# Optimization experiments

Hardware: AMD Instinct MI355X
Metric: run time of the kernel (lower is better)

## Reference

```python
import jax, jax.numpy as jnp
import numpy as np
import math

B, S, HID = 16, 1024, 1024
H, D = 16, 64  # heads, head_dim
WINDOW = 512  # pos bias length = 2*WINDOW+1 = 1025


def setup_inputs() -> dict:
    key = jax.random.key(0)
    ks = jax.random.split(key, 12)
    xav = lambda k, shp: jax.random.uniform(k, shp, jnp.float32, -1.0, 1.0) * math.sqrt(6.0 / (shp[0] + shp[1]))
    return {
        "hidden_states": jax.random.normal(ks[0], (B, S, HID), jnp.float32),
        "Wq": xav(ks[1], (HID, HID)), "bq": jnp.zeros((HID,), jnp.float32),
        "Wk": xav(ks[2], (HID, HID)), "bk": jnp.zeros((HID,), jnp.float32),
        "Wv": xav(ks[3], (HID, HID)), "bv": jnp.zeros((HID,), jnp.float32),
        "Wo": xav(ks[4], (HID, HID)), "bo": jnp.zeros((HID,), jnp.float32),
        "W_pe": xav(ks[5], (HID, 1)), "b_pe": jnp.zeros((HID,), jnp.float32),
        "pos_bias": 0.02 * jax.random.normal(ks[6], (1, H, 1, 2 * WINDOW + 1), jnp.float32),
        "clip_info": 0,
    }


def reference(hidden_states, Wq, bq, Wk, bk, Wv, bv, Wo, bo, W_pe, b_pe, pos_bias, clip_info):
    b, s, hid = hidden_states.shape
    mid = s // 2
    # relative positions in [-1, 1), shape [s, 1]
    positions = ((jnp.arange(s) - mid).astype(jnp.float32) / (mid + 1e-6))[:, None]
    pos_emb = positions @ W_pe.T + b_pe  # [s, hid]
    hs = hidden_states + pos_emb

    def heads(x):
        return x.reshape(b, s, H, D).transpose(0, 2, 1, 3)  # [b, H, s, D]

    q = heads(hs @ Wq.T + bq)
    k = heads(hs @ Wk.T + bk)
    v = heads(hs @ Wv.T + bv)

    scores = jnp.einsum("bhqd,bhkd->bhqk", q, k) / math.sqrt(D)
    scores = scores + pos_bias[:, :, :, :s]  # broadcast learned window bias over batch and query
    probs = jax.nn.softmax(scores, axis=-1)  # dropout is identity in eval mode
    ctx = jnp.einsum("bhqk,bhkd->bhqd", probs, v)
    ctx = ctx.transpose(0, 2, 1, 3).reshape(b, s, hid)
    return ctx @ Wo.T + bo
```

## Files before the change

kernel.cpp:

```cpp
#include <hip/hip_runtime.h>
#include <hip/hip_bf16.h>
#include <stdint.h>

#define BATCH 16
#define SEQ   1024
#define HIDN  1024
#define NH    16
#define HD    64
#define PBSTRIDE 1025

#define TS  64
#define AST 76

#define KSCL 0.18033688f
#define L2E  1.44269504f
#define MSUB 11.54156032f

#if __has_builtin(__builtin_amdgcn_exp2f)
#define EXP2(x) __builtin_amdgcn_exp2f(x)
#else
#define EXP2(x) exp2f(x)
#endif

typedef __attribute__((ext_vector_type(8))) short short8;
typedef __attribute__((ext_vector_type(4))) short short4v;
typedef __attribute__((ext_vector_type(4))) float f32x4;

__device__ __forceinline__ float bf2f(short x) {
    unsigned int u = ((unsigned int)(unsigned short)x) << 16;
    union { unsigned int u; float f; } c; c.u = u; return c.f;
}
__device__ __forceinline__ short f2bf(float f) {
    union { float f; unsigned int u; } c; c.f = f;
    unsigned int r = c.u + 0x7FFFu + ((c.u >> 16) & 1u);
    return (short)(r >> 16);
}
__device__ __forceinline__ short f2bf_fast(float f) {
    __hip_bfloat16 h = __float2bfloat16(f);
    return *reinterpret_cast<short*>(&h);
}

typedef __attribute__((address_space(1))) void gvoid;
typedef __attribute__((address_space(3))) void svoid;
__device__ __forceinline__ void gload_lds16(const void* g, void* l) {
    __builtin_amdgcn_global_load_lds((gvoid*)g, (svoid*)l, 16, 0, 0);
}

__global__ void convw4_k(const float* __restrict__ s0, const float* __restrict__ s1,
                         const float* __restrict__ s2, const float* __restrict__ s3,
                         short* __restrict__ d0, short* __restrict__ d1,
                         short* __restrict__ d2, short* __restrict__ d3) {
    const float* src = (blockIdx.y == 0) ? s0 : (blockIdx.y == 1) ? s1 : (blockIdx.y == 2) ? s2 : s3;
    short* dst       = (blockIdx.y == 0) ? d0 : (blockIdx.y == 1) ? d1 : (blockIdx.y == 2) ? d2 : d3;
    const float scl  = (blockIdx.y == 1) ? KSCL : 1.0f;
    int i = (blockIdx.x * 256 + threadIdx.x) * 4;
    float4 f = *(const float4*)(src + i);
    short4v o;
    o[0] = f2bf(f.x * scl); o[1] = f2bf(f.y * scl); o[2] = f2bf(f.z * scl); o[3] = f2bf(f.w * scl);
    *(short4v*)(dst + i) = o;
}

__global__ void convb_k(const float* __restrict__ b0, const float* __restrict__ b1,
                        const float* __restrict__ b2, float* __restrict__ fb) {
    int i = blockIdx.x * 256 + threadIdx.x;
    const float* s = (i < 1024) ? b0 : (i < 2048) ? b1 : b2;
    float scl = (i >= 1024 && i < 2048) ? KSCL : 1.0f;
    fb[i] = s[i & 1023] * scl;
}

__global__ void posemb_k(const float* __restrict__ hid, const float* __restrict__ wpe,
                         const float* __restrict__ bpe, short* __restrict__ hs) {
    long long idx = (long long)blockIdx.x * blockDim.x + threadIdx.x;
    long long base = idx * 8;
    int c = (int)(base & (HIDN - 1));
    int s = (int)((base >> 10) & (SEQ - 1));
    float pos = (float)(s - 512) * (1.0f / 512.0f);
    float4 h0 = *(const float4*)(hid + base);
    float4 h1 = *(const float4*)(hid + base + 4);
    float4 w0 = *(const float4*)(wpe + c);
    float4 w1 = *(const float4*)(wpe + c + 4);
    float4 b0 = *(const float4*)(bpe + c);
    float4 b1 = *(const float4*)(bpe + c + 4);
    short8 ov;
    ov[0] = f2bf(h0.x + pos * w0.x + b0.x);
    ov[1] = f2bf(h0.y + pos * w0.y + b0.y);
    ov[2] = f2bf(h0.z + pos * w0.z + b0.z);
    ov[3] = f2bf(h0.w + pos * w0.w + b0.w);
    ov[4] = f2bf(h1.x + pos * w1.x + b1.x);
    ov[5] = f2bf(h1.y + pos * w1.y + b1.y);
    ov[6] = f2bf(h1.z + pos * w1.z + b1.z);
    ov[7] = f2bf(h1.w + pos * w1.w + b1.w);
    *(short8*)(hs + base) = ov;
}

__global__ __launch_bounds__(256) void gemm_qkv(const short* __restrict__ A,
                                                const short* __restrict__ W,
                                                const float* __restrict__ fb,
                                                short* __restrict__ q,
                                                short* __restrict__ k,
                                                short* __restrict__ vt) {
    __shared__ __align__(16) short Als[128 * 64];
    __shared__ __align__(16) short Bls[128 * 64];
    const int tid  = threadIdx.x;
    const int lane = tid & 63;
    const int w    = tid >> 6;
    const int wr   = w >> 1, wc = w & 1;
    const int d0   = blockIdx.x;
    const int xcd  = d0 & 7;
    const int idx  = d0 >> 3;
    const int tx   = idx >> 4;
    const int ty   = xcd * 16 + (idx & 15);
    const int tm   = ty * 128;
    const int tn   = tx * 128;

    f32x4 acc[4][4] = {};

    const int srow = w * 32 + (lane >> 3);
    const int scol = ((lane & 7) ^ (lane >> 3)) * 8;
    const long long a_base = (long long)(tm + srow) * 1024 + scol;
    const long long b_base = (long long)(tn + srow) * 1024 + scol;
    char* alds = (char*)Als + w * 4096;
    char* blds = (char*)Bls + w * 4096;

    const int fr  = lane & 15;
    const int fg8 = (lane >> 4) * 8;
    const int frx = (lane & 7) * 8;

    for (int k0 = 0; k0 < 1024; k0 += 64) {
#pragma unroll
        for (int c = 0; c < 4; ++c) {
            gload_lds16((const void*)(A + a_base + (long long)c * 8 * 1024 + k0), alds + c * 1024);
            gload_lds16((const void*)(W + b_base + (long long)c * 8 * 1024 + k0), blds + c * 1024);
        }
        __syncthreads();
#pragma unroll
        for (int ks = 0; ks < 2; ++ks) {
            short8 af[4], bfr[4];
#pragma unroll
            for (int r = 0; r < 4; ++r) {
                af[r]  = *(const short8*)(Als + (wr * 64 + r * 16 + fr) * 64 + ((ks * 32 + fg8) ^ frx));
                bfr[r] = *(const short8*)(Bls + (wc * 64 + r * 16 + fr) * 64 + ((ks * 32 + fg8) ^ frx));
            }
#pragma unroll
            for (int mi = 0; mi < 4; ++mi)
#pragma unroll
                for (int ni = 0; ni < 4; ++ni)
                    acc[mi][ni] = __builtin_amdgcn_mfma_f32_16x16x32_bf16(af[mi], bfr[ni], acc[mi][ni], 0, 0, 0);
        }
        __syncthreads();
    }

    const int which = tn >> 10;
    short* dst = (which == 0) ? q : (which == 1) ? k : vt;
    const int g4 = (lane >> 4) * 4;
#pragma unroll
    for (int ni = 0; ni < 4; ++ni) {
        int col = tn + wc * 64 + ni * 16 + fr;
        int cc  = col & 1023;
        int h   = cc >> 6, d = cc & 63;
        float bv = fb[col];
#pragma unroll
        for (int mi = 0; mi < 4; ++mi) {
#pragma unroll
            for (int r = 0; r < 4; ++r) {
                int row = tm + wr * 64 + mi * 16 + g4 + r;
                int b = row >> 10, s = row & 1023;
                short o = f2bf(acc[mi][ni][r] + bv);
                if (which < 2)
                    dst[(((long long)(b * NH + h) * SEQ + s) << 6) + d] = o;
                else
                    dst[((long long)(b * NH + h) * HD + d) * SEQ + s] = o;
            }
        }
    }
}

__global__ __launch_bounds__(256) void gemm_out(const short* __restrict__ A,
                                                const short* __restrict__ W,
                                                const float* __restrict__ bias,
                                                float* __restrict__ Cout) {
    __shared__ __align__(16) short Als[128 * 64];
    __shared__ __align__(16) short Bls[128 * 64];
    const int tid  = threadIdx.x;
    const int lane = tid & 63;
    const int w    = tid >> 6;
    const int wr   = w >> 1, wc = w & 1;
    const int d0   = blockIdx.x;
    const int xcd  = d0 & 7;
    const int idx  = d0 >> 3;
    const int tx   = idx >> 4;
    const int ty   = xcd * 16 + (idx & 15);
    const int tm   = ty * 128;
    const int tn   = tx * 128;

    f32x4 acc[4][4] = {};

    const int srow = w * 32 + (lane >> 3);
    const int scol = ((lane & 7) ^ (lane >> 3)) * 8;
    const long long a_base = (long long)(tm + srow) * 1024 + scol;
    const long long b_base = (long long)(tn + srow) * 1024 + scol;
    char* alds = (char*)Als + w * 4096;
    char* blds = (char*)Bls + w * 4096;

    const int fr  = lane & 15;
    const int fg8 = (lane >> 4) * 8;
    const int frx = (lane & 7) * 8;

    for (int k0 = 0; k0 < 1024; k0 += 64) {
#pragma unroll
        for (int c = 0; c < 4; ++c) {
            gload_lds16((const void*)(A + a_base + (long long)c * 8 * 1024 + k0), alds + c * 1024);
            gload_lds16((const void*)(W + b_base + (long long)c * 8 * 1024 + k0), blds + c * 1024);
        }
        __syncthreads();
#pragma unroll
        for (int ks = 0; ks < 2; ++ks) {
            short8 af[4], bfr[4];
#pragma unroll
            for (int r = 0; r < 4; ++r) {
                af[r]  = *(const short8*)(Als + (wr * 64 + r * 16 + fr) * 64 + ((ks * 32 + fg8) ^ frx));
                bfr[r] = *(const short8*)(Bls + (wc * 64 + r * 16 + fr) * 64 + ((ks * 32 + fg8) ^ frx));
            }
#pragma unroll
            for (int mi = 0; mi < 4; ++mi)
#pragma unroll
                for (int ni = 0; ni < 4; ++ni)
                    acc[mi][ni] = __builtin_amdgcn_mfma_f32_16x16x32_bf16(af[mi], bfr[ni], acc[mi][ni], 0, 0, 0);
        }
        __syncthreads();
    }

    const int g4 = (lane >> 4) * 4;
#pragma unroll
    for (int ni = 0; ni < 4; ++ni) {
        int col = tn + wc * 64 + ni * 16 + fr;
        float bv = bias[col];
#pragma unroll
        for (int mi = 0; mi < 4; ++mi)
#pragma unroll
            for (int r = 0; r < 4; ++r) {
                int row = tm + wr * 64 + mi * 16 + g4 + r;
                Cout[(long long)row * 1024 + col] = acc[mi][ni][r] + bv;
            }
    }
}

__global__ __launch_bounds__(256) void attn_k(const short* __restrict__ Q,
                                              const short* __restrict__ Kg,
                                              const short* __restrict__ Vt,
                                              const float* __restrict__ pbias,
                                              short* __restrict__ ctx) {
    __shared__ __align__(16) short Kls[2][64 * TS];
    __shared__ __align__(16) short Vls[2][64 * TS];
    __shared__ __align__(16) short Pls[4 * 32 * AST];

    const int tid  = threadIdx.x;
    const int lane = tid & 63;
    const int w    = tid >> 6;
    const int d0   = blockIdx.x;
    const int bh   = (d0 & 7) * 32 + (d0 >> 6);
    const int qt   = (d0 >> 3) & 7;
    const int h    = bh & (NH - 1);
    const long long base = (long long)bh * (SEQ * HD);

    const int fr = lane & 15;
    const int fg = lane >> 4;

    const int trow = w * 16 + (lane >> 3);
    const int scol = ((lane & 7) ^ (lane >> 3)) * 8;
    const int ldso = w * 1024;
    const long long kg0 = base + (long long)trow * HD + scol;
    const long long vg0 = base + (long long)trow * SEQ + scol;

    short8 qf[2][2];
#pragma unroll
    for (int mi = 0; mi < 2; ++mi)
#pragma unroll
        for (int ks = 0; ks < 2; ++ks)
            qf[mi][ks] = *(const short8*)(Q + base + (long long)(qt * 128 + w * 32 + mi * 16 + fr) * HD + ks * 32 + fg * 8);

    f32x4 o[2][4] = {};
    f32x4 osum[2] = {};
    short8 vones;
#pragma unroll
    for (int j = 0; j < 8; ++j) vones[j] = (short)0x3F80;

    short* Pw = Pls + w * 32 * AST;
    const float* pbh = pbias + h * PBSTRIDE;
    const int swc = (fr & 7) << 3;

    {
        const short* ks0 = Kg + kg0;
        const short* vs0 = Vt + vg0;
        gload_lds16(ks0,           Kls[0] + ldso);
        gload_lds16(ks0 + 8 * HD,  Kls[0] + ldso + 512);
        gload_lds16(vs0,           Vls[0] + ldso);
        gload_lds16(vs0 + 8 * SEQ, Vls[0] + ldso + 512);
    }
    float pbm[4];
#pragma unroll
    for (int ni = 0; ni < 4; ++ni)
        pbm[ni] = fmaf(pbh[ni * 16 + fr], L2E, -MSUB);
    asm volatile("s_waitcnt vmcnt(0)" ::: "memory");
    __syncthreads();

    int cur = 0;
    for (int kt = 0; kt < 16; ++kt) {
        if (kt < 15) {
            const int nb = cur ^ 1;
            const short* ks0 = Kg + kg0 + (long long)((kt + 1) * 64) * HD;
            const short* vs0 = Vt + vg0 + (kt + 1) * 64;
            gload_lds16(ks0,           Kls[nb] + ldso);
            gload_lds16(ks0 + 8 * HD,  Kls[nb] + ldso + 512);
            gload_lds16(vs0,           Vls[nb] + ldso);
            gload_lds16(vs0 + 8 * SEQ, Vls[nb] + ldso + 512);
        }

        f32x4 sc[2][4];
#pragma unroll
        for (int mi = 0; mi < 2; ++mi)
#pragma unroll
            for (int ni = 0; ni < 4; ++ni)
                sc[mi][ni] = (f32x4){pbm[ni], pbm[ni], pbm[ni], pbm[ni]};
        __builtin_amdgcn_s_setprio(1);
#pragma unroll
        for (int ks = 0; ks < 2; ++ks) {
#pragma unroll
            for (int ni = 0; ni < 4; ++ni) {
                short8 kb = *(const short8*)(Kls[cur] + (ni * 16 + fr) * TS + ((ks * 32 + fg * 8) ^ swc));
#pragma unroll
                for (int mi = 0; mi < 2; ++mi)
                    sc[mi][ni] = __builtin_amdgcn_mfma_f32_16x16x32_bf16(qf[mi][ks], kb, sc[mi][ni], 0, 0, 0);
            }
        }
        __builtin_amdgcn_s_setprio(0);

#pragma unroll
        for (int mi = 0; mi < 2; ++mi)
#pragma unroll
            for (int ni = 0; ni < 4; ++ni)
#pragma unroll
                for (int r = 0; r < 4; ++r)
                    Pw[(mi * 16 + fg * 4 + r) * AST + ni * 16 + fr] =
                        f2bf_fast(EXP2(sc[mi][ni][r]));

        {
            const int nkt = (kt + 1) & 15;
#pragma unroll
            for (int ni = 0; ni < 4; ++ni)
                pbm[ni] = fmaf(pbh[nkt * 64 + ni * 16 + fr], L2E, -MSUB);
        }

        __builtin_amdgcn_s_setprio(1);
#pragma unroll
        for (int ks = 0; ks < 2; ++ks) {
            short8 pa[2];
#pragma unroll
            for (int mi = 0; mi < 2; ++mi)
                pa[mi] = *(const short8*)(Pw + (mi * 16 + fr) * AST + ks * 32 + fg * 8);
            osum[0] = __builtin_amdgcn_mfma_f32_16x16x32_bf16(pa[0], vones, osum[0], 0, 0, 0);
            osum[1] = __builtin_amdgcn_mfma_f32_16x16x32_bf16(pa[1], vones, osum[1], 0, 0, 0);
#pragma unroll
            for (int di = 0; di < 4; ++di) {
                short8 vb = *(const short8*)(Vls[cur] + (di * 16 + fr) * TS + ((ks * 32 + fg * 8) ^ swc));
#pragma unroll
                for (int mi = 0; mi < 2; ++mi)
                    o[mi][di] = __builtin_amdgcn_mfma_f32_16x16x32_bf16(pa[mi], vb, o[mi][di], 0, 0, 0);
            }
        }
        __builtin_amdgcn_s_setprio(0);

        asm volatile("s_waitcnt vmcnt(0)" ::: "memory");
        __syncthreads();
        cur ^= 1;
    }

    const int b = bh >> 4;
#pragma unroll
    for (int mi = 0; mi < 2; ++mi) {
#pragma unroll
        for (int r = 0; r < 4; ++r) {
            float inv = 1.0f / osum[mi][r];
            int srow = qt * 128 + w * 32 + mi * 16 + fg * 4 + r;
#pragma unroll
            for (int di = 0; di < 4; ++di) {
                int d = di * 16 + fr;
                ctx[(long long)(b * SEQ + srow) * HIDN + h * HD + d] = f2bf(o[mi][di][r] * inv);
            }
        }
    }
}

extern "C" void kernel_launch(void* const* d_in, const int* in_sizes, int n_in,
                              void* d_out, int out_size, void* d_ws, size_t ws_size,
                              hipStream_t stream) {
    const float* hid  = (const float*)d_in[0];
    const float* Wq   = (const float*)d_in[1];
    const float* bq   = (const float*)d_in[2];
    const float* Wk   = (const float*)d_in[3];
    const float* bk   = (const float*)d_in[4];
    const float* Wv   = (const float*)d_in[5];
    const float* bv   = (const float*)d_in[6];
    const float* Wo   = (const float*)d_in[7];
    const float* bo   = (const float*)d_in[8];
    const float* Wpe  = (const float*)d_in[9];
    const float* bpe  = (const float*)d_in[10];
    const float* pbias = (const float*)d_in[11];

    const long long NE = (long long)BATCH * SEQ * HIDN;
    const long long WSZ = (long long)HIDN * HIDN;

    short* hs   = (short*)d_ws;
    short* vt   = hs + NE;
    short* Wcq  = vt + NE;
    short* Wck  = Wcq + WSZ;
    short* Wcv  = Wck + WSZ;
    short* Wco  = Wcv + WSZ;
    float* fb   = (float*)(Wco + WSZ);
    short* q    = (short*)d_out;
    short* k    = q + NE;
    short* ctx  = hs;

    posemb_k<<<(int)(NE / 8 / 256), 256, 0, stream>>>(hid, Wpe, bpe, hs);
    convw4_k<<<dim3((int)(WSZ / 4 / 256), 4), 256, 0, stream>>>(Wq, Wk, Wv, Wo, Wcq, Wck, Wcv, Wco);
    convb_k<<<12, 256, 0, stream>>>(bq, bk, bv, fb);

    gemm_qkv<<<3072, 256, 0, stream>>>(hs, Wcq, fb, q, k, vt);

    attn_k<<<2048, 256, 0, stream>>>(q, k, vt, pbias, ctx);

    gemm_out<<<1024, 256, 0, stream>>>(ctx, Wco, bo, (float*)d_out);
}
```

Before: 352.5 us.

## Double-buffer LDS tiles in QKV and output GEMMs; vectorize V-transpose store

Both projection GEMMs now allocate two LDS buffers per operand. They prefetch the next K-tile via global-to-LDS loads while MFMAs run on the current tile, so load latency overlaps compute instead of being serialized behind a barrier. The QKV epilogue is split by destination, and the transposed V output now writes four consecutive sequence elements as one packed store instead of scalar stores. LDS use per block doubles, which can lower occupancy. Correctness relies on the barrier at the end of each iteration also draining the outstanding async loads.

Result: faster. 338.2 us (-4.1%).

```diff
diff --git a/kernel.cpp b/kernel.cpp
--- a/kernel.cpp
+++ b/kernel.cpp
@@ -99,8 +99,8 @@
                                                 short* __restrict__ q,
                                                 short* __restrict__ k,
                                                 short* __restrict__ vt) {
-    __shared__ __align__(16) short Als[128 * 64];
-    __shared__ __align__(16) short Bls[128 * 64];
+    __shared__ __align__(16) short Als[2][128 * 64];
+    __shared__ __align__(16) short Bls[2][128 * 64];
     const int tid  = threadIdx.x;
     const int lane = tid & 63;
     const int w    = tid >> 6;
@@ -119,27 +119,39 @@
     const int scol = ((lane & 7) ^ (lane >> 3)) * 8;
     const long long a_base = (long long)(tm + srow) * 1024 + scol;
     const long long b_base = (long long)(tn + srow) * 1024 + scol;
-    char* alds = (char*)Als + w * 4096;
-    char* blds = (char*)Bls + w * 4096;
+    const int ldsw = w * 4096;
 
     const int fr  = lane & 15;
     const int fg8 = (lane >> 4) * 8;
     const int frx = (lane & 7) * 8;
 
+#pragma unroll
+    for (int c = 0; c < 4; ++c) {
+        gload_lds16((const void*)(A + a_base + (long long)c * 8 * 1024), (char*)Als[0] + ldsw + c * 1024);
+        gload_lds16((const void*)(W + b_base + (long long)c * 8 * 1024), (char*)Bls[0] + ldsw + c * 1024);
+    }
+    asm volatile("s_waitcnt vmcnt(0)" ::: "memory");
+    __syncthreads();
+
+    int cur = 0;
     for (int k0 = 0; k0 < 1024; k0 += 64) {
-#pragma unroll
-        for (int c = 0; c < 4; ++c) {
-            gload_lds16((const void*)(A + a_base + (long long)c * 8 * 1024 + k0), alds + c * 1024);
-            gload_lds16((const void*)(W + b_base + (long long)c * 8 * 1024 + k0), blds + c * 1024);
-        }
-        __syncthreads();
+        if (k0 + 64 < 1024) {
+            const int nb = cur ^ 1;
+#pragma unroll
+            for (int c = 0; c < 4; ++c) {
+                gload_lds16((const void*)(A + a_base + (long long)c * 8 * 1024 + k0 + 64),
+                            (char*)Als[nb] + ldsw + c * 1024);
+                gload_lds16((const void*)(W + b_base + (long long)c * 8 * 1024 + k0 + 64),
+                            (char*)Bls[nb] + ldsw + c * 1024);
+            }
+        }
 #pragma unroll
         for (int ks = 0; ks < 2; ++ks) {
             short8 af[4], bfr[4];
 #pragma unroll
             for (int r = 0; r < 4; ++r) {
-                af[r]  = *(const short8*)(Als + (wr * 64 + r * 16 + fr) * 64 + ((ks * 32 + fg8) ^ frx));
-                bfr[r] = *(const short8*)(Bls + (wc * 64 + r * 16 + fr) * 64 + ((ks * 32 + fg8) ^ frx));
+                af[r]  = *(const short8*)(Als[cur] + (wr * 64 + r * 16 + fr) * 64 + ((ks * 32 + fg8) ^ frx));
+                bfr[r] = *(const short8*)(Bls[cur] + (wc * 64 + r * 16 + fr) * 64 + ((ks * 32 + fg8) ^ frx));
             }
 #pragma unroll
             for (int mi = 0; mi < 4; ++mi)
@@ -148,28 +160,44 @@
                     acc[mi][ni] = __builtin_amdgcn_mfma_f32_16x16x32_bf16(af[mi], bfr[ni], acc[mi][ni], 0, 0, 0);
         }
         __syncthreads();
+        cur ^= 1;
     }
 
     const int which = tn >> 10;
-    short* dst = (which == 0) ? q : (which == 1) ? k : vt;
     const int g4 = (lane >> 4) * 4;
-#pragma unroll
-    for (int ni = 0; ni < 4; ++ni) {
-        int col = tn + wc * 64 + ni * 16 + fr;
-        int cc  = col & 1023;
-        int h   = cc >> 6, d = cc & 63;
-        float bv = fb[col];
-#pragma unroll
-        for (int mi = 0; mi < 4; ++mi) {
-#pragma unroll
-            for (int r = 0; r < 4; ++r) {
-                int row = tm + wr * 64 + mi * 16 + g4 + r;
-                int b = row >> 10, s = row & 1023;
-                short o = f2bf(acc[mi][ni][r] + bv);
-                if (which < 2)
-                    dst[(((long long)(b * NH + h) * SEQ + s) << 6) + d] = o;
-                else
-                    dst[((long long)(b * NH + h) * HD + d) * SEQ + s] = o;
+    if (which < 2) {
+        short* dst = (which == 0) ? q : k;
+#pragma unroll
+        for (int ni = 0; ni < 4; ++ni) {
+            int col = tn + wc * 64 + ni * 16 + fr;
+            int cc  = col & 1023;
+            int h   = cc >> 6, d = cc & 63;
+            float bv = fb[col];
+#pragma unroll
+            for (int mi = 0; mi < 4; ++mi) {
+#pragma unroll
+                for (int r = 0; r < 4; ++r) {
+                    int row = tm + wr * 64 + mi * 16 + g4 + r;
+                    int b = row >> 10, s = row & 1023;
+                    dst[(((long long)(b * NH + h) * SEQ + s) << 6) + d] = f2bf(acc[mi][ni][r] + bv);
+                }
+            }
+        }
+    } else {
+#pragma unroll
+        for (int ni = 0; ni < 4; ++ni) {
+            int col = tn + wc * 64 + ni * 16 + fr;
+            int cc  = col & 1023;
+            int h   = cc >> 6, d = cc & 63;
+            float bv = fb[col];
+#pragma unroll
+            for (int mi = 0; mi < 4; ++mi) {
+                int row0 = tm + wr * 64 + mi * 16 + g4;
+                int b = row0 >> 10, s0 = row0 & 1023;
+                short4v o4;
+#pragma unroll
+                for (int r = 0; r < 4; ++r) o4[r] = f2bf(acc[mi][ni][r] + bv);
+                *(short4v*)(vt + ((long long)(b * NH + h) * HD + d) * SEQ + s0) = o4;
             }
         }
     }
@@ -179,8 +207,8 @@
                                                 const short* __restrict__ W,
                                                 const float* __restrict__ bias,
                                                 float* __restrict__ Cout) {
-    __shared__ __align__(16) short Als[128 * 64];
-    __shared__ __align__(16) short Bls[128 * 64];
+    __shared__ __align__(16) short Als[2][128 * 64];
+    __shared__ __align__(16) short Bls[2][128 * 64];
     const int tid  = threadIdx.x;
     const int lane = tid & 63;
     const int w    = tid >> 6;
@@ -199,27 +227,39 @@
     const int scol = ((lane & 7) ^ (lane >> 3)) * 8;
     const long long a_base = (long long)(tm + srow) * 1024 + scol;
     const long long b_base = (long long)(tn + srow) * 1024 + scol;
-    char* alds = (char*)Als + w * 4096;
-    char* blds = (char*)Bls + w * 4096;
+    const int ldsw = w * 4096;
 
     const int fr  = lane & 15;
     const int fg8 = (lane >> 4) * 8;
     const int frx = (lane & 7) * 8;
 
+#pragma unroll
+    for (int c = 0; c < 4; ++c) {
+        gload_lds16((const void*)(A + a_base + (long long)c * 8 * 1024), (char*)Als[0] + ldsw + c * 1024);
+        gload_lds16((const void*)(W + b_base + (long long)c * 8 * 1024), (char*)Bls[0] + ldsw + c * 1024);
+    }
+    asm volatile("s_waitcnt vmcnt(0)" ::: "memory");
+    __syncthreads();
+
+    int cur = 0;
     for (int k0 = 0; k0 < 1024; k0 += 64) {
-#pragma unroll
-        for (int c = 0; c < 4; ++c) {
-            gload_lds16((const void*)(A + a_base + (long long)c * 8 * 1024 + k0), alds + c * 1024);
-            gload_lds16((const void*)(W + b_base + (long long)c * 8 * 1024 + k0), blds + c * 1024);
-        }
-        __syncthreads();
+        if (k0 + 64 < 1024) {
+            const int nb = cur ^ 1;
+#pragma unroll
+            for (int c = 0; c < 4; ++c) {
+                gload_lds16((const void*)(A + a_base + (long long)c * 8 * 1024 + k0 + 64),
+                            (char*)Als[nb] + ldsw + c * 1024);
+                gload_lds16((const void*)(W + b_base + (long long)c * 8 * 1024 + k0 + 64),
+                            (char*)Bls[nb] + ldsw + c * 1024);
+            }
+        }
 #pragma unroll
         for (int ks = 0; ks < 2; ++ks) {
             short8 af[4], bfr[4];
 #pragma unroll
             for (int r = 0; r < 4; ++r) {
-                af[r]  = *(const short8*)(Als + (wr * 64 + r * 16 + fr) * 64 + ((ks * 32 + fg8) ^ frx));
-                bfr[r] = *(const short8*)(Bls + (wc * 64 + r * 16 + fr) * 64 + ((ks * 32 + fg8) ^ frx));
+                af[r]  = *(const short8*)(Als[cur] + (wr * 64 + r * 16 + fr) * 64 + ((ks * 32 + fg8) ^ frx));
+                bfr[r] = *(const short8*)(Bls[cur] + (wc * 64 + r * 16 + fr) * 64 + ((ks * 32 + fg8) ^ frx));
             }
 #pragma unroll
             for (int mi = 0; mi < 4; ++mi)
@@ -228,6 +268,7 @@
                     acc[mi][ni] = __builtin_amdgcn_mfma_f32_16x16x32_bf16(af[mi], bfr[ni], acc[mi][ni], 0, 0, 0);
         }
         __syncthreads();
+        cur ^= 1;
     }
 
     const int g4 = (lane >> 4) * 4;
```
